# Optimization experiments

Measured on AMD Instinct MI355X. Metric: run time of the kernel, lower is better.

## Reference

```python
import jax, jax.numpy as jnp
from jax import lax
import numpy as np

T = 64          # psum accumulation length (input elements per partial sum)
NBITS_ACC = 8   # accumulator bit width
Q = 2 ** (NBITS_ACC - 1)  # signed clip range [-Q, Q-1]


def _binarize(x):
    """sign() binarization with straight-through estimator (hardtanh grad)."""
    xc = jnp.clip(x, -1.0, 1.0)
    return xc + lax.stop_gradient(jnp.sign(x) - xc)


def _binconv3x3(x, w, stride=1):
    """Binarized 3x3 conv with digital partial-sum clipping.

    Both activations and weights are binarized to {-1,0,+1} via sign. The
    reduction over Cin*3*3 is split into chunks of T elements; each chunk's
    partial sum is saturated to the nbits_acc-bit signed accumulator range
    before being added to the running total (digital psum scheme).
    """
    xb = _binarize(x)
    wb = _binarize(w)
    O, C, KH, KW = w.shape
    # patches: [N, C*KH*KW, Ho, Wo], feature dim ordered (C, KH, KW)
    patches = lax.conv_general_dilated_patches(
        xb, (KH, KW), (stride, stride), ((1, 1), (1, 1)))
    N, R, Ho, Wo = patches.shape
    G = R // T  # number of psum chunks (2304 / 64 = 36)
    p = patches.reshape(N, G, T, Ho, Wo).transpose(1, 0, 2, 3, 4)  # [G,N,T,H,W]
    wr = wb.reshape(O, G, T).transpose(1, 0, 2)                    # [G,O,T]

    def step(acc, gt):
        pg, wg = gt
        ps = jnp.einsum('nthw,ot->nohw', pg, wg)   # chunk partial sum
        ps = jnp.clip(ps, -float(Q), float(Q - 1))  # accumulator saturation
        return acc + ps, None

    init = jnp.zeros((N, O, Ho, Wo), x.dtype)
    out, _ = lax.scan(step, init, (p, wr))
    return out


def _bn(x, gamma, beta, eps=1e-5):
    # training-mode BatchNorm2d: batch statistics over (N, H, W)
    m = x.mean((0, 2, 3), keepdims=True)
    v = ((x - m) ** 2).mean((0, 2, 3), keepdims=True)
    return (x - m) / jnp.sqrt(v + eps) * gamma[None, :, None, None] + beta[None, :, None, None]


def setup_inputs() -> dict:
    key = jax.random.key(0)
    ks = jax.random.split(key, 3)
    N, C, H, W = 32, 256, 28, 28
    x = jax.random.normal(ks[0], (N, C, H, W), dtype=jnp.float32)
    w1 = jax.random.normal(ks[1], (C, C, 3, 3), dtype=jnp.float32) * 0.05
    w2 = jax.random.normal(ks[2], (C, C, 3, 3), dtype=jnp.float32) * 0.05
    return {
        'x': x,
        'w1': w1,
        'bn1_gamma': jnp.ones((C,), jnp.float32),
        'bn1_beta': jnp.zeros((C,), jnp.float32),
        'w2': w2,
        'bn2_gamma': jnp.ones((C,), jnp.float32),
        'bn2_beta': jnp.zeros((C,), jnp.float32),
    }


def reference(x, w1, bn1_gamma, bn1_beta, w2, bn2_gamma, bn2_beta):
    residual = x
    out = _binconv3x3(x, w1, stride=1)
    out = _bn(out, bn1_gamma, bn1_beta)
    out = jnp.clip(out, -1.0, 1.0)          # Hardtanh
    out = _binconv3x3(out, w2, stride=1)
    out = out + residual                    # identity residual (no downsample)
    out = _bn(out, bn2_gamma, bn2_beta)     # do_bntan=True
    out = jnp.clip(out, -1.0, 1.0)          # Hardtanh
    return out
```

## Files before the change

kernel.cpp:

```cpp
#include <hip/hip_runtime.h>
#include <stdint.h>

typedef unsigned long long u64;

#define NN 32
#define CC 256
#define HH 28
#define WW 28
#define PP 784
#define NHW 25088
#define WPO 36

__global__ __launch_bounds__(64) void prep(const float* __restrict__ x,
        const float* __restrict__ w1, const float* __restrict__ w2,
        u64* __restrict__ xp, u64* __restrict__ wp1, u64* __restrict__ wp2,
        int* s1i, u64* s1q, double* s2s, double* s2q) {
    int bx = blockIdx.x, lane = threadIdx.x;
    if (bx < 1664) {
        int n = bx / 52, rem = bx % 52, g = rem / 13, pt = rem % 13;
        int p = pt * 64 + lane;
        if (p < PP) {
            const float* base = x + ((size_t)n * CC + g * 64) * PP + p;
            u64 w = 0;
#pragma unroll 8
            for (int cb = 0; cb < 64; ++cb)
                if (base[(size_t)cb * PP] > 0.0f) w |= (1ull << cb);
            xp[((size_t)n * PP + p) * 4 + g] = w;
        }
    } else {
        int u = bx - 1664, which = u >> 8, o = u & 255;
        if (u < 4) {
            s1i[u * 64 + lane] = 0; s1q[u * 64 + lane] = 0ull;
            s2s[u * 64 + lane] = 0.0; s2q[u * 64 + lane] = 0.0;
        }
        const float* w = which ? w2 : w1;
        u64* wp = which ? wp2 : wp1;
#pragma unroll
        for (int cg = 0; cg < 4; ++cg)
            for (int tap = 0; tap < 9; ++tap) {
                u64 m = __ballot(w[((size_t)o * CC + cg * 64 + lane) * 9 + tap] > 0.0f);
                if (lane == 0) wp[(size_t)o * WPO + tap * 4 + cg] = m;
            }
    }
}


#define POPW(acc, T, wb) acc = (int)__popcll((T) ^ wreg[wb]) + acc;
#define POP4(acc, T, WB) { POPW(acc, T[0], (WB)+0) POPW(acc, T[1], (WB)+1) \
                           POPW(acc, T[2], (WB)+2) POPW(acc, T[3], (WB)+3) }

#define LOADROW(T, lr, ccc) { \
    ulonglong2 u0 = *(const ulonglong2*)&lin[lr][ccc][0]; \
    ulonglong2 u1 = *(const ulonglong2*)&lin[lr][ccc][2]; \
    T[0] = u0.x; T[1] = u0.y; T[2] = u1.x; T[3] = u1.y; }

#define COLBODY(ccc, AP, AC, AN) { \
    u64 t0[4], t1[4], t2[4]; \
    LOADROW(t1, wid + 1, ccc) \
    if (rtop) { LOADROW(t0, wid, ccc) } \
    if (rbot) { LOADROW(t2, wid + 2, ccc) } \
    if (rtop) { POP4(AN, t0, 0)  POP4(AC, t0, 4)  POP4(AP, t0, 8)  } \
    POP4(AN, t1, 12) POP4(AC, t1, 16) POP4(AP, t1, 20) \
    if (rbot) { POP4(AN, t2, 24) POP4(AC, t2, 28) POP4(AP, t2, 32) } }

#define EMIT(emc, A) { \
    int K = ((emc) == 0 || (emc) == 27) ? bb2 : bb3; \
    int dot = K - 2 * (A); \
    *vptr = (short)dot; vptr += CC; \
    if (MODE == 0) { tsi += dot; tqi += dot * dot; } \
    else { float u = (float)dot + resrow[emc]; tsf += u; tqf = fmaf(u, u, tqf); } }

template<int MODE>
__global__ __attribute__((amdgpu_flat_work_group_size(128, 128), amdgpu_waves_per_eu(3, 4)))
void binconv(const u64* __restrict__ xp, const u64* __restrict__ wp,
             short* __restrict__ vout, const float* __restrict__ xres,
             int* __restrict__ s_i, u64* __restrict__ s_q,
             double* __restrict__ s2s, double* __restrict__ s2q)
{
    __shared__ u64 lin[4][28][4];
    __shared__ double reds[2][64];
    __shared__ double redq[2][64];

    int tid = threadIdx.x, lane = tid & 63, wid = tid >> 6;
    int rt = blockIdx.x, ob = blockIdx.y, n = blockIdx.z;
    int r0 = rt * 2;
    int o = ob * 64 + lane;

    for (int idx = tid; idx < 4 * 56; idx += 128) {
        int row = idx / 56, off = idx % 56;
        int gr = r0 - 1 + row;
        if (gr >= 0 && gr < HH) {
            ulonglong2 t = *(const ulonglong2*)(xp + ((size_t)n * PP + gr * WW) * 4 + off * 2);
            *(ulonglong2*)((u64*)lin + row * 112 + off * 2) = t;
        }
    }

    u64 wreg[36];
    {
        const ulonglong2* wv = (const ulonglong2*)(wp + (size_t)o * WPO);
#pragma unroll
        for (int k = 0; k < 18; ++k) { ulonglong2 t = wv[k]; wreg[2*k] = t.x; wreg[2*k+1] = t.y; }
    }
    asm volatile("" : "+v"(wreg[0]), "+v"(wreg[1]), "+v"(wreg[2]), "+v"(wreg[3]),
                      "+v"(wreg[4]), "+v"(wreg[5]), "+v"(wreg[6]), "+v"(wreg[7]),
                      "+v"(wreg[8]), "+v"(wreg[9]), "+v"(wreg[10]), "+v"(wreg[11]),
                      "+v"(wreg[12]), "+v"(wreg[13]), "+v"(wreg[14]), "+v"(wreg[15]),
                      "+v"(wreg[16]), "+v"(wreg[17]));
    asm volatile("" : "+v"(wreg[18]), "+v"(wreg[19]), "+v"(wreg[20]), "+v"(wreg[21]),
                      "+v"(wreg[22]), "+v"(wreg[23]), "+v"(wreg[24]), "+v"(wreg[25]),
                      "+v"(wreg[26]), "+v"(wreg[27]), "+v"(wreg[28]), "+v"(wreg[29]),
                      "+v"(wreg[30]), "+v"(wreg[31]), "+v"(wreg[32]), "+v"(wreg[33]),
                      "+v"(wreg[34]), "+v"(wreg[35]));
    __syncthreads();

    int r = r0 + wid;
    const bool rtop = (r > 0), rbot = (r < HH - 1);
    const int nr = 1 + (int)rtop + (int)rbot;
    const int bb3 = 256 * nr * 3, bb2 = 256 * nr * 2;

    short* vptr = vout + ((size_t)n * PP + (size_t)r * WW) * CC + o;
    const float* resrow = (MODE == 1) ? (xres + ((size_t)n * CC + o) * PP + r * WW) : nullptr;

    int tsi = 0, tqi = 0; float tsf = 0.0f, tqf = 0.0f;
    int a = 0, b = 0, c = 0;

    {
        u64 t0[4], t1[4], t2[4];
        LOADROW(t1, wid + 1, 0)
        if (rtop) { LOADROW(t0, wid, 0) }
        if (rbot) { LOADROW(t2, wid + 2, 0) }
        if (rtop) { POP4(c, t0, 0)  POP4(b, t0, 4)  }
        POP4(c, t1, 12) POP4(b, t1, 16)
        if (rbot) { POP4(c, t2, 24) POP4(b, t2, 28) }
    }

#pragma unroll 1
    for (int m = 0; m < 9; ++m) {
        int cc = 3 * m + 1;
        COLBODY(cc,     b, c, a)  EMIT(cc - 1, b)  b = 0;
        COLBODY(cc + 1, c, a, b)  EMIT(cc,     c)  c = 0;
        COLBODY(cc + 2, a, b, c)  EMIT(cc + 1, a)  a = 0;
    }
    EMIT(27, b)

    reds[wid][lane] = (MODE == 0) ? (double)tsi : (double)tsf;
    redq[wid][lane] = (MODE == 0) ? (double)tqi : (double)tqf;
    __syncthreads();
    if (wid == 0) {
        double S = reds[0][lane] + reds[1][lane];
        double Q = redq[0][lane] + redq[1][lane];
        if (MODE == 0) {
            atomicAdd(&s_i[o], (int)S);
            atomicAdd(&s_q[o], (u64)(long long)Q);
        } else {
            atomicAdd(&s2s[o], S);
            atomicAdd(&s2q[o], Q);
        }
    }
}

__global__ __launch_bounds__(256) void repack(const short* __restrict__ v1,
                                              const int* __restrict__ s_i, const u64* __restrict__ s_q,
                                              const float* __restrict__ gamma, const float* __restrict__ beta,
                                              u64* __restrict__ xp2) {
    int pt = blockIdx.x, n = blockIdx.y;
    int tid = threadIdx.x, lane = tid & 63, g = tid >> 6;
    int c = tid;
    double mean = (double)s_i[c] * (1.0 / NHW);
    double msq  = (double)s_q[c] * (1.0 / NHW);
    double var  = msq - mean * mean;
    double istd = 1.0 / sqrt(var + 1e-5);
    double ad   = (double)gamma[c] * istd;
    float a = (float)ad;
    float b = (float)((double)beta[c] - mean * ad);
#pragma unroll
    for (int i = 0; i < 16; ++i) {
        int p = pt * 16 + i;
        int v = v1[((size_t)n * PP + p) * CC + c];
        u64 m = __ballot(fmaf(a, (float)v, b) > 0.0f);
        if (lane == 0) xp2[((size_t)n * PP + p) * 4 + g] = m;
    }
}

__global__ __launch_bounds__(256) void finalize(const short* __restrict__ v2, const float* __restrict__ x,
                                                const double* __restrict__ s2s, const double* __restrict__ s2q,
                                                const float* __restrict__ gamma, const float* __restrict__ beta,
                                                float* __restrict__ out) {
    __shared__ short t[64 * 66];
    __shared__ float scs[64], bis[64];
    int ct = blockIdx.x, pt = blockIdx.y, n = blockIdx.z;
    int p0 = pt * 64, c0 = ct * 64;
    int tid = threadIdx.x;
    if (tid < 64) {
        int c = c0 + tid;
        double mean = s2s[c] * (1.0 / NHW);
        double msq  = s2q[c] * (1.0 / NHW);
        double var  = msq - mean * mean;
        double istd = 1.0 / sqrt(var + 1e-5);
        double ad   = (double)gamma[c] * istd;
        scs[tid] = (float)ad;
        bis[tid] = (float)((double)beta[c] - mean * ad);
    }
    for (int idx = tid; idx < 64 * 64; idx += 256) {
        int i = idx >> 6, j = idx & 63;
        int p = p0 + i;
        if (p < PP) t[i * 66 + j] = v2[((size_t)n * PP + p) * CC + c0 + j];
    }
    __syncthreads();
    int pl = tid & 63;
    int p = p0 + pl;
    if (p < PP) {
        for (int cl = tid >> 6; cl < 64; cl += 4) {
            int c = c0 + cl;
            float val = (float)t[pl * 66 + cl] + x[((size_t)n * CC + c) * PP + p];
            float r = fmaf(scs[cl], val, bis[cl]);
            r = fminf(fmaxf(r, -1.0f), 1.0f);
            out[((size_t)n * CC + c) * PP + p] = r;
        }
    }
}

extern "C" void kernel_launch(void* const* d_in, const int* in_sizes, int n_in,
                              void* d_out, int out_size, void* d_ws, size_t ws_size,
                              hipStream_t stream) {
    (void)in_sizes; (void)n_in; (void)out_size; (void)ws_size;
    const float* x   = (const float*)d_in[0];
    const float* w1  = (const float*)d_in[1];
    const float* g1  = (const float*)d_in[2];
    const float* b1  = (const float*)d_in[3];
    const float* w2  = (const float*)d_in[4];
    const float* g2  = (const float*)d_in[5];
    const float* b2  = (const float*)d_in[6];
    float* out = (float*)d_out;

    char* ws = (char*)d_ws;
    u64*    xp1 = (u64*)(ws + 0);
    u64*    xp2 = (u64*)(ws + 802816);
    u64*    wp1 = (u64*)(ws + 1605632);
    u64*    wp2 = (u64*)(ws + 1679360);
    int*    s1i = (int*)(ws + 1753088);
    u64*    s1q = (u64*)(ws + 1754112);
    double* s2s = (double*)(ws + 1756160);
    double* s2q = (double*)(ws + 1758208);
    short*  v12 = (short*)(ws + 1764352);

    prep<<<2176, 64, 0, stream>>>(x, w1, w2, xp1, wp1, wp2, s1i, s1q, s2s, s2q);
    binconv<0><<<dim3(14, 4, 32), 128, 0, stream>>>(xp1, wp1, v12, nullptr, s1i, s1q, nullptr, nullptr);
    repack<<<dim3(49, 32), 256, 0, stream>>>(v12, s1i, s1q, g1, b1, xp2);
    binconv<1><<<dim3(14, 4, 32), 128, 0, stream>>>(xp2, wp2, v12, x, nullptr, nullptr, s2s, s2q);
    finalize<<<dim3(4, 13, 32), 256, 0, stream>>>(v12, x, s2s, s2q, g2, b2, out);
}
```

Before: 123.7 us.

## Restructure binconv to per-pixel threads with NCHW output and separate stats kernels

The binary conv now assigns one pixel per thread, holding its 3x3x256-bit window in registers. It loops over 32 output channels whose weight words are read with uniform (scalar) loads. Border handling moves to a per-channel padding-correction table built in prep, and results are written in NCHW layout. BatchNorm statistics move from atomics inside the conv into dedicated stats1/stats2 reduction kernels, and repack/finalize are rewritten for the new layout, with finalize vectorised. This trades the sliding-window register reuse for simpler coalesced stores, at the cost of two extra kernel launches and extra passes over the intermediate buffer.

```diff
diff --git a/kernel.cpp b/kernel.cpp
--- a/kernel.cpp
+++ b/kernel.cpp
@@ -3,7 +3,6 @@
 
 typedef unsigned long long u64;
 
-#define NN 32
 #define CC 256
 #define HH 28
 #define WW 28
@@ -14,7 +13,8 @@
 __global__ __launch_bounds__(64) void prep(const float* __restrict__ x,
         const float* __restrict__ w1, const float* __restrict__ w2,
         u64* __restrict__ xp, u64* __restrict__ wp1, u64* __restrict__ wp2,
-        int* s1i, u64* s1q, double* s2s, double* s2q) {
+        int* __restrict__ dt1, int* __restrict__ dt2,
+        int* s1i, double* s1q, double* s2s, double* s2q) {
     int bx = blockIdx.x, lane = threadIdx.x;
     if (bx < 1664) {
         int n = bx / 52, rem = bx % 52, g = rem / 13, pt = rem % 13;
@@ -30,194 +30,198 @@
     } else {
         int u = bx - 1664, which = u >> 8, o = u & 255;
         if (u < 4) {
-            s1i[u * 64 + lane] = 0; s1q[u * 64 + lane] = 0ull;
+            s1i[u * 64 + lane] = 0; s1q[u * 64 + lane] = 0.0;
             s2s[u * 64 + lane] = 0.0; s2q[u * 64 + lane] = 0.0;
         }
         const float* w = which ? w2 : w1;
         u64* wp = which ? wp2 : wp1;
+        int* dt = which ? dt2 : dt1;
+        __shared__ u64 wsm[36];
 #pragma unroll
         for (int cg = 0; cg < 4; ++cg)
             for (int tap = 0; tap < 9; ++tap) {
                 u64 m = __ballot(w[((size_t)o * CC + cg * 64 + lane) * 9 + tap] > 0.0f);
-                if (lane == 0) wp[(size_t)o * WPO + tap * 4 + cg] = m;
+                if (lane == 0) { wp[(size_t)o * WPO + tap * 4 + cg] = m; wsm[tap * 4 + cg] = m; }
             }
-    }
-}
-
-
-#define POPW(acc, T, wb) acc = (int)__popcll((T) ^ wreg[wb]) + acc;
-#define POP4(acc, T, WB) { POPW(acc, T[0], (WB)+0) POPW(acc, T[1], (WB)+1) \
-                           POPW(acc, T[2], (WB)+2) POPW(acc, T[3], (WB)+3) }
-
-#define LOADROW(T, lr, ccc) { \
-    ulonglong2 u0 = *(const ulonglong2*)&lin[lr][ccc][0]; \
-    ulonglong2 u1 = *(const ulonglong2*)&lin[lr][ccc][2]; \
-    T[0] = u0.x; T[1] = u0.y; T[2] = u1.x; T[3] = u1.y; }
-
-#define COLBODY(ccc, AP, AC, AN) { \
-    u64 t0[4], t1[4], t2[4]; \
-    LOADROW(t1, wid + 1, ccc) \
-    if (rtop) { LOADROW(t0, wid, ccc) } \
-    if (rbot) { LOADROW(t2, wid + 2, ccc) } \
-    if (rtop) { POP4(AN, t0, 0)  POP4(AC, t0, 4)  POP4(AP, t0, 8)  } \
-    POP4(AN, t1, 12) POP4(AC, t1, 16) POP4(AP, t1, 20) \
-    if (rbot) { POP4(AN, t2, 24) POP4(AC, t2, 28) POP4(AP, t2, 32) } }
-
-#define EMIT(emc, A) { \
-    int K = ((emc) == 0 || (emc) == 27) ? bb2 : bb3; \
-    int dot = K - 2 * (A); \
-    *vptr = (short)dot; vptr += CC; \
-    if (MODE == 0) { tsi += dot; tqi += dot * dot; } \
-    else { float u = (float)dot + resrow[emc]; tsf += u; tqf = fmaf(u, u, tqf); } }
-
-template<int MODE>
-__global__ __attribute__((amdgpu_flat_work_group_size(128, 128), amdgpu_waves_per_eu(3, 4)))
+        __syncthreads();
+        if (lane == 0) {
+            int tp[9];
+#pragma unroll
+            for (int t = 0; t < 9; ++t)
+                tp[t] = (int)__popcll(wsm[t*4]) + (int)__popcll(wsm[t*4+1])
+                      + (int)__popcll(wsm[t*4+2]) + (int)__popcll(wsm[t*4+3]);
+            for (int e = 0; e < 16; ++e) {
+                int C = 0, np = 0;
+                for (int t = 0; t < 9; ++t) {
+                    int tr = t / 3, tc = t % 3;
+                    bool pad = ((e & 1) && tr == 0) || ((e & 2) && tr == 2)
+                            || ((e & 4) && tc == 0) || ((e & 8) && tc == 2);
+                    if (pad) { C += tp[t]; np++; }
+                }
+                dt[o * 16 + e] = 2 * C - 256 * np;
+            }
+        }
+    }
+}
+
+__global__ __attribute__((amdgpu_flat_work_group_size(64, 64), amdgpu_waves_per_eu(4, 4)))
 void binconv(const u64* __restrict__ xp, const u64* __restrict__ wp,
-             short* __restrict__ vout, const float* __restrict__ xres,
-             int* __restrict__ s_i, u64* __restrict__ s_q,
-             double* __restrict__ s2s, double* __restrict__ s2q)
-{
-    __shared__ u64 lin[4][28][4];
-    __shared__ double reds[2][64];
-    __shared__ double redq[2][64];
-
-    int tid = threadIdx.x, lane = tid & 63, wid = tid >> 6;
-    int rt = blockIdx.x, ob = blockIdx.y, n = blockIdx.z;
-    int r0 = rt * 2;
-    int o = ob * 64 + lane;
-
-    for (int idx = tid; idx < 4 * 56; idx += 128) {
+             const int* __restrict__ dtab, short* __restrict__ vout) {
+    __shared__ u64 lin[6][30][4];
+    __shared__ int dl[512];
+    int lane = threadIdx.x;
+    int pt = blockIdx.x, og = blockIdx.y, n = blockIdx.z;
+    int p0 = pt * 64;
+    int rf = p0 / 28;
+    int rl = (p0 + 63) / 28; if (rl > 27) rl = 27;
+
+    for (int i = lane; i < 720; i += 64) ((u64*)lin)[i] = 0;
+    __syncthreads();
+    int nrows = rl - rf + 3;
+    for (int idx = lane; idx < nrows * 56; idx += 64) {
         int row = idx / 56, off = idx % 56;
-        int gr = r0 - 1 + row;
+        int gr = rf - 1 + row;
         if (gr >= 0 && gr < HH) {
             ulonglong2 t = *(const ulonglong2*)(xp + ((size_t)n * PP + gr * WW) * 4 + off * 2);
-            *(ulonglong2*)((u64*)lin + row * 112 + off * 2) = t;
-        }
-    }
-
-    u64 wreg[36];
+            *(ulonglong2*)((u64*)lin + (size_t)row * 120 + 4 + off * 2) = t;
+        }
+    }
+    for (int j = lane; j < 512; j += 64) dl[j] = dtab[og * 512 + j];
+    __syncthreads();
+
+    int p = p0 + lane;
+    bool st = (p < PP);
+    int pc = st ? p : (PP - 1);
+    int r = pc / 28, c = pc % 28;
+    int lrow = r - rf + 1;
+
+    u64 win[36];
+#pragma unroll
+    for (int dr = 0; dr < 3; ++dr)
+#pragma unroll
+        for (int dc = 0; dc < 3; ++dc) {
+            const u64* q = &lin[lrow - 1 + dr][c + dc][0];
+            ulonglong2 q0 = *(const ulonglong2*)q;
+            ulonglong2 q1 = *(const ulonglong2*)(q + 2);
+            int t = (dr * 3 + dc) * 4;
+            win[t] = q0.x; win[t + 1] = q0.y; win[t + 2] = q1.x; win[t + 3] = q1.y;
+        }
+    int eidx = (r == 0 ? 1 : 0) | (r == 27 ? 2 : 0) | (c == 0 ? 4 : 0) | (c == 27 ? 8 : 0);
+
+    short* vp = vout + ((size_t)n * CC + og * 32) * PP + p;
+#pragma unroll 1
+    for (int i = 0; i < 32; ++i) {
+        const u64* wo = wp + (size_t)(og * 32 + i) * WPO;
+        int a0 = 0, a1 = 0, a2 = 0, a3 = 0;
+#pragma unroll
+        for (int t = 0; t < 9; ++t) {
+            a0 += (int)__popcll(win[t*4+0] ^ wo[t*4+0]);
+            a1 += (int)__popcll(win[t*4+1] ^ wo[t*4+1]);
+            a2 += (int)__popcll(win[t*4+2] ^ wo[t*4+2]);
+            a3 += (int)__popcll(win[t*4+3] ^ wo[t*4+3]);
+        }
+        int dot = 2304 + dl[i * 16 + eidx] - 2 * (a0 + a1 + a2 + a3);
+        if (st) *vp = (short)dot;
+        vp += PP;
+    }
+}
+
+__global__ __launch_bounds__(256) void stats1(const short* __restrict__ v1,
+                                              int* __restrict__ s1i, double* __restrict__ s1q) {
+    int o = blockIdx.x, nq = blockIdx.y, tid = threadIdx.x;
+    int s = 0, q = 0;
+    for (int nn = 0; nn < 8; ++nn) {
+        const short* b = v1 + ((size_t)(nq * 8 + nn) * CC + o) * PP;
+        for (int j = tid; j < PP; j += 256) { int v = b[j]; s += v; q += v * v; }
+    }
+    double qd = (double)q;
+    for (int d = 32; d; d >>= 1) { s += __shfl_down(s, d, 64); qd += __shfl_down(qd, d, 64); }
+    __shared__ int rs[4]; __shared__ double rq[4];
+    int wid = tid >> 6;
+    if ((tid & 63) == 0) { rs[wid] = s; rq[wid] = qd; }
+    __syncthreads();
+    if (tid == 0) {
+        atomicAdd(&s1i[o], rs[0] + rs[1] + rs[2] + rs[3]);
+        atomicAdd(&s1q[o], rq[0] + rq[1] + rq[2] + rq[3]);
+    }
+}
+
+__global__ __launch_bounds__(256) void repack(const short* __restrict__ v1,
+        const int* __restrict__ s1i, const double* __restrict__ s1q,
+        const float* __restrict__ gamma, const float* __restrict__ beta,
+        u64* __restrict__ xp2) {
+    __shared__ float ash[256], bsh[256];
+    int pt = blockIdx.x, n = blockIdx.y, tid = threadIdx.x;
     {
-        const ulonglong2* wv = (const ulonglong2*)(wp + (size_t)o * WPO);
-#pragma unroll
-        for (int k = 0; k < 18; ++k) { ulonglong2 t = wv[k]; wreg[2*k] = t.x; wreg[2*k+1] = t.y; }
-    }
-    asm volatile("" : "+v"(wreg[0]), "+v"(wreg[1]), "+v"(wreg[2]), "+v"(wreg[3]),
-                      "+v"(wreg[4]), "+v"(wreg[5]), "+v"(wreg[6]), "+v"(wreg[7]),
-                      "+v"(wreg[8]), "+v"(wreg[9]), "+v"(wreg[10]), "+v"(wreg[11]),
-                      "+v"(wreg[12]), "+v"(wreg[13]), "+v"(wreg[14]), "+v"(wreg[15]),
-                      "+v"(wreg[16]), "+v"(wreg[17]));
-    asm volatile("" : "+v"(wreg[18]), "+v"(wreg[19]), "+v"(wreg[20]), "+v"(wreg[21]),
-                      "+v"(wreg[22]), "+v"(wreg[23]), "+v"(wreg[24]), "+v"(wreg[25]),
-                      "+v"(wreg[26]), "+v"(wreg[27]), "+v"(wreg[28]), "+v"(wreg[29]),
-                      "+v"(wreg[30]), "+v"(wreg[31]), "+v"(wreg[32]), "+v"(wreg[33]),
-                      "+v"(wreg[34]), "+v"(wreg[35]));
-    __syncthreads();
-
-    int r = r0 + wid;
-    const bool rtop = (r > 0), rbot = (r < HH - 1);
-    const int nr = 1 + (int)rtop + (int)rbot;
-    const int bb3 = 256 * nr * 3, bb2 = 256 * nr * 2;
-
-    short* vptr = vout + ((size_t)n * PP + (size_t)r * WW) * CC + o;
-    const float* resrow = (MODE == 1) ? (xres + ((size_t)n * CC + o) * PP + r * WW) : nullptr;
-
-    int tsi = 0, tqi = 0; float tsf = 0.0f, tqf = 0.0f;
-    int a = 0, b = 0, c = 0;
-
-    {
-        u64 t0[4], t1[4], t2[4];
-        LOADROW(t1, wid + 1, 0)
-        if (rtop) { LOADROW(t0, wid, 0) }
-        if (rbot) { LOADROW(t2, wid + 2, 0) }
-        if (rtop) { POP4(c, t0, 0)  POP4(b, t0, 4)  }
-        POP4(c, t1, 12) POP4(b, t1, 16)
-        if (rbot) { POP4(c, t2, 24) POP4(b, t2, 28) }
-    }
-
-#pragma unroll 1
-    for (int m = 0; m < 9; ++m) {
-        int cc = 3 * m + 1;
-        COLBODY(cc,     b, c, a)  EMIT(cc - 1, b)  b = 0;
-        COLBODY(cc + 1, c, a, b)  EMIT(cc,     c)  c = 0;
-        COLBODY(cc + 2, a, b, c)  EMIT(cc + 1, a)  a = 0;
-    }
-    EMIT(27, b)
-
-    reds[wid][lane] = (MODE == 0) ? (double)tsi : (double)tsf;
-    redq[wid][lane] = (MODE == 0) ? (double)tqi : (double)tqf;
-    __syncthreads();
-    if (wid == 0) {
-        double S = reds[0][lane] + reds[1][lane];
-        double Q = redq[0][lane] + redq[1][lane];
-        if (MODE == 0) {
-            atomicAdd(&s_i[o], (int)S);
-            atomicAdd(&s_q[o], (u64)(long long)Q);
-        } else {
-            atomicAdd(&s2s[o], S);
-            atomicAdd(&s2q[o], Q);
-        }
-    }
-}
-
-__global__ __launch_bounds__(256) void repack(const short* __restrict__ v1,
-                                              const int* __restrict__ s_i, const u64* __restrict__ s_q,
-                                              const float* __restrict__ gamma, const float* __restrict__ beta,
-                                              u64* __restrict__ xp2) {
-    int pt = blockIdx.x, n = blockIdx.y;
-    int tid = threadIdx.x, lane = tid & 63, g = tid >> 6;
-    int c = tid;
-    double mean = (double)s_i[c] * (1.0 / NHW);
-    double msq  = (double)s_q[c] * (1.0 / NHW);
+        int cc = tid;
+        double mean = (double)s1i[cc] * (1.0 / NHW);
+        double msq  = s1q[cc] * (1.0 / NHW);
+        double var  = msq - mean * mean;
+        double istd = 1.0 / sqrt(var + 1e-5);
+        double ad   = (double)gamma[cc] * istd;
+        ash[cc] = (float)ad;
+        bsh[cc] = (float)((double)beta[cc] - mean * ad);
+    }
+    __syncthreads();
+    int g = tid >> 6, lane = tid & 63;
+    int p = pt * 64 + lane;
+    bool act = p < PP;
+    int pcl = act ? p : PP - 1;
+    u64 wbits = 0;
+#pragma unroll 8
+    for (int cb = 0; cb < 64; ++cb) {
+        int cc = g * 64 + cb;
+        int v = v1[((size_t)n * CC + cc) * PP + pcl];
+        float y = fmaf(ash[cc], (float)v, bsh[cc]);
+        if (y > 0.0f) wbits |= (1ull << cb);
+    }
+    if (act) xp2[((size_t)n * PP + p) * 4 + g] = wbits;
+}
+
+__global__ __launch_bounds__(256) void stats2(const short* __restrict__ v2, const float* __restrict__ x,
+                                              double* __restrict__ s2s, double* __restrict__ s2q) {
+    int o = blockIdx.x, nq = blockIdx.y, tid = threadIdx.x;
+    double sd = 0.0, qd = 0.0;
+    for (int nn = 0; nn < 8; ++nn) {
+        size_t base = ((size_t)(nq * 8 + nn) * CC + o) * PP;
+        for (int j = tid; j < PP; j += 256) {
+            float u = (float)v2[base + j] + x[base + j];
+            sd += (double)u; qd += (double)u * (double)u;
+        }
+    }
+    for (int d = 32; d; d >>= 1) { sd += __shfl_down(sd, d, 64); qd += __shfl_down(qd, d, 64); }
+    __shared__ double rs[4], rq[4];
+    int wid = tid >> 6;
+    if ((tid & 63) == 0) { rs[wid] = sd; rq[wid] = qd; }
+    __syncthreads();
+    if (tid == 0) {
+        atomicAdd(&s2s[o], rs[0] + rs[1] + rs[2] + rs[3]);
+        atomicAdd(&s2q[o], rq[0] + rq[1] + rq[2] + rq[3]);
+    }
+}
+
+__global__ __launch_bounds__(256) void finalize(const short* __restrict__ v2, const float* __restrict__ x,
+        const double* __restrict__ s2s, const double* __restrict__ s2q,
+        const float* __restrict__ gamma, const float* __restrict__ beta,
+        float* __restrict__ out) {
+    int i4 = blockIdx.x * 256 + threadIdx.x;
+    size_t flat = (size_t)i4 * 4;
+    int cc = (int)((flat / PP) & 255);
+    double mean = s2s[cc] * (1.0 / NHW);
+    double msq  = s2q[cc] * (1.0 / NHW);
     double var  = msq - mean * mean;
     double istd = 1.0 / sqrt(var + 1e-5);
-    double ad   = (double)gamma[c] * istd;
-    float a = (float)ad;
-    float b = (float)((double)beta[c] - mean * ad);
-#pragma unroll
-    for (int i = 0; i < 16; ++i) {
-        int p = pt * 16 + i;
-        int v = v1[((size_t)n * PP + p) * CC + c];
-        u64 m = __ballot(fmaf(a, (float)v, b) > 0.0f);
-        if (lane == 0) xp2[((size_t)n * PP + p) * 4 + g] = m;
-    }
-}
-
-__global__ __launch_bounds__(256) void finalize(const short* __restrict__ v2, const float* __restrict__ x,
-                                                const double* __restrict__ s2s, const double* __restrict__ s2q,
-                                                const float* __restrict__ gamma, const float* __restrict__ beta,
-                                                float* __restrict__ out) {
-    __shared__ short t[64 * 66];
-    __shared__ float scs[64], bis[64];
-    int ct = blockIdx.x, pt = blockIdx.y, n = blockIdx.z;
-    int p0 = pt * 64, c0 = ct * 64;
-    int tid = threadIdx.x;
-    if (tid < 64) {
-        int c = c0 + tid;
-        double mean = s2s[c] * (1.0 / NHW);
-        double msq  = s2q[c] * (1.0 / NHW);
-        double var  = msq - mean * mean;
-        double istd = 1.0 / sqrt(var + 1e-5);
-        double ad   = (double)gamma[c] * istd;
-        scs[tid] = (float)ad;
-        bis[tid] = (float)((double)beta[c] - mean * ad);
-    }
-    for (int idx = tid; idx < 64 * 64; idx += 256) {
-        int i = idx >> 6, j = idx & 63;
-        int p = p0 + i;
-        if (p < PP) t[i * 66 + j] = v2[((size_t)n * PP + p) * CC + c0 + j];
-    }
-    __syncthreads();
-    int pl = tid & 63;
-    int p = p0 + pl;
-    if (p < PP) {
-        for (int cl = tid >> 6; cl < 64; cl += 4) {
-            int c = c0 + cl;
-            float val = (float)t[pl * 66 + cl] + x[((size_t)n * CC + c) * PP + p];
-            float r = fmaf(scs[cl], val, bis[cl]);
-            r = fminf(fmaxf(r, -1.0f), 1.0f);
-            out[((size_t)n * CC + c) * PP + p] = r;
-        }
-    }
+    double ad   = (double)gamma[cc] * istd;
+    float sc = (float)ad;
+    float bi = (float)((double)beta[cc] - mean * ad);
+    float4 xv = *(const float4*)(x + flat);
+    short4 vv = *(const short4*)(v2 + flat);
+    float4 ov;
+    ov.x = fminf(fmaxf(fmaf(sc, (float)vv.x + xv.x, bi), -1.0f), 1.0f);
+    ov.y = fminf(fmaxf(fmaf(sc, (float)vv.y + xv.y, bi), -1.0f), 1.0f);
+    ov.z = fminf(fmaxf(fmaf(sc, (float)vv.z + xv.z, bi), -1.0f), 1.0f);
+    ov.w = fminf(fmaxf(fmaf(sc, (float)vv.w + xv.w, bi), -1.0f), 1.0f);
+    *(float4*)(out + flat) = ov;
 }
 
 extern "C" void kernel_launch(void* const* d_in, const int* in_sizes, int n_in,
@@ -239,14 +243,18 @@
     u64*    wp1 = (u64*)(ws + 1605632);
     u64*    wp2 = (u64*)(ws + 1679360);
     int*    s1i = (int*)(ws + 1753088);
-    u64*    s1q = (u64*)(ws + 1754112);
+    double* s1q = (double*)(ws + 1754112);
     double* s2s = (double*)(ws + 1756160);
     double* s2q = (double*)(ws + 1758208);
-    short*  v12 = (short*)(ws + 1764352);
-
-    prep<<<2176, 64, 0, stream>>>(x, w1, w2, xp1, wp1, wp2, s1i, s1q, s2s, s2q);
-    binconv<0><<<dim3(14, 4, 32), 128, 0, stream>>>(xp1, wp1, v12, nullptr, s1i, s1q, nullptr, nullptr);
-    repack<<<dim3(49, 32), 256, 0, stream>>>(v12, s1i, s1q, g1, b1, xp2);
-    binconv<1><<<dim3(14, 4, 32), 128, 0, stream>>>(xp2, wp2, v12, x, nullptr, nullptr, s2s, s2q);
-    finalize<<<dim3(4, 13, 32), 256, 0, stream>>>(v12, x, s2s, s2q, g2, b2, out);
-}
+    int*    dt1 = (int*)(ws + 1760256);
+    int*    dt2 = (int*)(ws + 1776640);
+    short*  v12 = (short*)(ws + 1793024);
+
+    prep<<<2176, 64, 0, stream>>>(x, w1, w2, xp1, wp1, wp2, dt1, dt2, s1i, s1q, s2s, s2q);
+    binconv<<<dim3(13, 8, 32), 64, 0, stream>>>(xp1, wp1, dt1, v12);
+    stats1<<<dim3(256, 4), 256, 0, stream>>>(v12, s1i, s1q);
+    repack<<<dim3(13, 32), 256, 0, stream>>>(v12, s1i, s1q, g1, b1, xp2);
+    binconv<<<dim3(13, 8, 32), 64, 0, stream>>>(xp2, wp2, dt2, v12);
+    stats2<<<dim3(256, 4), 256, 0, stream>>>(v12, x, s2s, s2q);
+    finalize<<<6272, 256, 0, stream>>>(v12, x, s2s, s2q, g2, b2, out);
+}
```

Measured after the change: 154.8 us. 1.25x slower.
